# Kernel optimization log

Hardware: AMD Instinct MI355X
Metric: run time of the kernel (lower is better)

The kernel has to match this reference:

```python
import jax, jax.numpy as jnp
import numpy as np


def setup_inputs() -> dict:
    key = jax.random.key(0)
    k1, _ = jax.random.split(key)
    x = jax.random.normal(k1, (32, 64, 192, 192), dtype=jnp.float32)
    gamma = jnp.zeros((1,), dtype=jnp.float32)
    return {"x": x, "gamma": gamma}


def reference(x, gamma):
    B, C, H, W = x.shape
    q = x.reshape(B, C, H * W)                      # [B, C, N]
    # energy[b, c, d] = <q[b,c,:], q[b,d,:]>
    energy = jnp.einsum('bcn,bdn->bcd', q, q)       # [B, C, C]
    # max-subtract trick: softmax over (max - energy)
    energy_new = jnp.max(energy, axis=-1, keepdims=True) - energy
    attention = jax.nn.softmax(energy_new, axis=-1)  # [B, C, C]
    out = jnp.einsum('bcd,bdn->bcn', attention, q)   # [B, C, N]
    out = out.reshape(B, C, H, W)
    return x * (gamma[0] * out) + x
```

## Files before the change

### kernel.cpp

```cpp
#include <hip/hip_runtime.h>


#define BATCH 32
#define CH 64
#define NSP 36864

#define KSPLIT 36
#define KPER (NSP / KSPLIT)
#define BK 64

#define NB 128

using frag  = __attribute__((ext_vector_type(8))) short;
using f32x4 = __attribute__((ext_vector_type(4))) float;

__device__ inline unsigned short f2bf(float f) {
    unsigned u = __builtin_bit_cast(unsigned, f);
    unsigned r = (u + 0x7FFFu + ((u >> 16) & 1u)) >> 16;
    return (unsigned short)r;
}
__device__ inline unsigned pack2(float a, float b) {
    return (unsigned)f2bf(a) | ((unsigned)f2bf(b) << 16);
}

__global__ __launch_bounds__(256) void gram_kernel(const float* __restrict__ x,
                                                   float* __restrict__ energy) {
    const int b = blockIdx.x;
    const int kb = blockIdx.y;
    const int tid = threadIdx.x;
    const int wv = tid >> 6;
    const int lane = tid & 63;
    const int l15 = lane & 15;
    const int quad = lane >> 4;

    __shared__ unsigned short tile[CH][72];

    const float* xb = x + (size_t)b * CH * NSP + (size_t)kb * KPER;

    f32x4 acc[4];
#pragma unroll
    for (int cb = 0; cb < 4; cb++)
#pragma unroll
        for (int r = 0; r < 4; r++) acc[cb][r] = 0.f;

    for (int s = 0; s < KPER / BK; s++) {
        float4 v[4];
#pragma unroll
        for (int rep = 0; rep < 4; rep++) {
            int idx = rep * 256 + tid;
            int c = idx >> 4, kq = idx & 15;
            v[rep] = *(const float4*)&xb[(size_t)c * NSP + s * BK + kq * 4];
        }
        __syncthreads();
#pragma unroll
        for (int rep = 0; rep < 4; rep++) {
            int idx = rep * 256 + tid;
            int c = idx >> 4, kq = idx & 15;
            uint2 p;
            p.x = pack2(v[rep].x, v[rep].y);
            p.y = pack2(v[rep].z, v[rep].w);
            *(uint2*)&tile[c][kq * 4] = p;
        }
        __syncthreads();

#pragma unroll
        for (int ks = 0; ks < 2; ks++) {
            frag a = *(const frag*)&tile[wv * 16 + l15][ks * 32 + quad * 8];
#pragma unroll
            for (int cb = 0; cb < 4; cb++) {
                frag bb = *(const frag*)&tile[cb * 16 + l15][ks * 32 + quad * 8];
                acc[cb] = __builtin_amdgcn_mfma_f32_16x16x32_bf16(a, bb, acc[cb], 0, 0, 0);
            }
        }
    }

    float* eb = energy + (size_t)b * CH * CH;
#pragma unroll
    for (int cb = 0; cb < 4; cb++)
#pragma unroll
        for (int r = 0; r < 4; r++) {
            int row = wv * 16 + quad * 4 + r;
            int col = cb * 16 + l15;
            atomicAdd(&eb[row * CH + col], acc[cb][r]);
        }
}

__global__ __launch_bounds__(64) void softmax_kernel(const float* __restrict__ energy,
                                                     float* __restrict__ att) {
    const int row = blockIdx.x;
    const int d = threadIdx.x;
    float e = energy[(size_t)row * CH + d];

    float m = e;
#pragma unroll
    for (int off = 32; off > 0; off >>= 1) m = fmaxf(m, __shfl_down(m, off));
    m = __shfl(m, 0);

    float en = m - e;

    float mx = en;
#pragma unroll
    for (int off = 32; off > 0; off >>= 1) mx = fmaxf(mx, __shfl_down(mx, off));
    mx = __shfl(mx, 0);

    float ex = __expf(en - mx);
    float s = ex;
#pragma unroll
    for (int off = 32; off > 0; off >>= 1) s += __shfl_down(s, off);
    s = __shfl(s, 0);

    att[(size_t)row * CH + d] = ex / s;
}

__global__ __launch_bounds__(256) void proj_kernel(const float* __restrict__ x,
                                                   const float* __restrict__ att,
                                                   const float* __restrict__ gamma,
                                                   float* __restrict__ out) {
    const int b = blockIdx.x;
    const int n0 = blockIdx.y * NB;
    const int tid = threadIdx.x;
    const int wv = tid >> 6;
    const int lane = tid & 63;
    const int l15 = lane & 15;
    const int quad = lane >> 4;

    __shared__ float xs[CH][NB + 1];
    __shared__ unsigned short satt[CH][72];

    const float* xb = x + (size_t)b * CH * NSP;

#pragma unroll
    for (int rep = 0; rep < 4; rep++) {
        int idx = rep * 256 + tid;
        int c = idx >> 4, j = idx & 15;
        float4 v = *(const float4*)&att[(size_t)b * CH * CH + c * CH + j * 4];
        uint2 p;
        p.x = pack2(v.x, v.y);
        p.y = pack2(v.z, v.w);
        *(uint2*)&satt[c][j * 4] = p;
    }
#pragma unroll
    for (int rep = 0; rep < 8; rep++) {
        int idx = rep * 256 + tid;
        int d = idx >> 5, nq = idx & 31;
        float4 v = *(const float4*)&xb[(size_t)d * NSP + n0 + nq * 4];
        *(float4*)&xs[d][nq * 4] = v;
    }
    __syncthreads();

    const float g = gamma[0];

    f32x4 acc[2][4];
#pragma unroll
    for (int t = 0; t < 2; t++)
#pragma unroll
        for (int cb = 0; cb < 4; cb++)
#pragma unroll
            for (int r = 0; r < 4; r++) acc[t][cb][r] = 0.f;

#pragma unroll
    for (int ks = 0; ks < 2; ks++) {
        frag af[4];
#pragma unroll
        for (int cb = 0; cb < 4; cb++)
            af[cb] = *(const frag*)&satt[cb * 16 + l15][ks * 32 + quad * 8];
#pragma unroll
        for (int t = 0; t < 2; t++) {
            int n = (wv * 2 + t) * 16 + l15;
            int k0 = ks * 32 + quad * 8;
            uint4 packed;
            packed.x = pack2(xs[k0 + 0][n], xs[k0 + 1][n]);
            packed.y = pack2(xs[k0 + 2][n], xs[k0 + 3][n]);
            packed.z = pack2(xs[k0 + 4][n], xs[k0 + 5][n]);
            packed.w = pack2(xs[k0 + 6][n], xs[k0 + 7][n]);
            frag bf = __builtin_bit_cast(frag, packed);
#pragma unroll
            for (int cb = 0; cb < 4; cb++)
                acc[t][cb] = __builtin_amdgcn_mfma_f32_16x16x32_bf16(af[cb], bf, acc[t][cb], 0, 0, 0);
        }
    }

    float* ob = out + (size_t)b * CH * NSP;
#pragma unroll
    for (int t = 0; t < 2; t++) {
        int n = (wv * 2 + t) * 16 + l15;
#pragma unroll
        for (int cb = 0; cb < 4; cb++)
#pragma unroll
            for (int r = 0; r < 4; r++) {
                int c = cb * 16 + quad * 4 + r;
                float xv = xs[c][n];
                ob[(size_t)c * NSP + n0 + n] = fmaf(xv * g, acc[t][cb][r], xv);
            }
    }
}

extern "C" void kernel_launch(void* const* d_in, const int* in_sizes, int n_in,
                              void* d_out, int out_size, void* d_ws, size_t ws_size,
                              hipStream_t stream) {
    const float* x = (const float*)d_in[0];
    const float* gamma = (const float*)d_in[1];
    float* out = (float*)d_out;

    float* energy = (float*)d_ws;
    float* att = energy + (size_t)BATCH * CH * CH;

    hipMemsetAsync(energy, 0, (size_t)BATCH * CH * CH * sizeof(float), stream);

    gram_kernel<<<dim3(BATCH, KSPLIT), 256, 0, stream>>>(x, energy);
    softmax_kernel<<<BATCH * CH, 64, 0, stream>>>(energy, att);
    proj_kernel<<<dim3(BATCH, NSP / NB), 256, 0, stream>>>(x, att, gamma, out);
}
```

Before: 598.8 us.

## Prefetch next tiles in gram and proj kernels, replace atomics with partial buffers

The gram kernel doubles its K tile and loads the next tile into registers while MFMAs run on the current one. It writes per-split partial Gram matrices instead of using atomicAdd, which removes the memset; the softmax kernel sums the 36 partials. The proj kernel now walks 8 spatial chunks per block with register prefetch of the next chunk, and both kernels get occupancy hints in launch_bounds. In exchange the workspace is larger, softmax does more reads, and there is more register pressure.

```diff
diff --git a/kernel.cpp b/kernel.cpp
--- a/kernel.cpp
+++ b/kernel.cpp
@@ -7,9 +7,12 @@
 
 #define KSPLIT 36
 #define KPER (NSP / KSPLIT)
-#define BK 64
+#define BK 128
+#define SITER (KPER / BK)
 
 #define NB 128
+#define NCHUNK 8
+#define NBLKY (NSP / (NB * NCHUNK))
 
 using frag  = __attribute__((ext_vector_type(8))) short;
 using f32x4 = __attribute__((ext_vector_type(4))) float;
@@ -23,8 +26,8 @@
     return (unsigned)f2bf(a) | ((unsigned)f2bf(b) << 16);
 }
 
-__global__ __launch_bounds__(256) void gram_kernel(const float* __restrict__ x,
-                                                   float* __restrict__ energy) {
+__global__ __launch_bounds__(256, 4) void gram_kernel(const float* __restrict__ x,
+                                                      float* __restrict__ part) {
     const int b = blockIdx.x;
     const int kb = blockIdx.y;
     const int tid = threadIdx.x;
@@ -33,7 +36,7 @@
     const int l15 = lane & 15;
     const int quad = lane >> 4;
 
-    __shared__ unsigned short tile[CH][72];
+    __shared__ unsigned short tile[CH][BK + 8];
 
     const float* xb = x + (size_t)b * CH * NSP + (size_t)kb * KPER;
 
@@ -43,19 +46,20 @@
 #pragma unroll
         for (int r = 0; r < 4; r++) acc[cb][r] = 0.f;
 
-    for (int s = 0; s < KPER / BK; s++) {
-        float4 v[4];
-#pragma unroll
-        for (int rep = 0; rep < 4; rep++) {
+    float4 v[8];
+#pragma unroll
+    for (int rep = 0; rep < 8; rep++) {
+        int idx = rep * 256 + tid;
+        int c = idx >> 5, kq = idx & 31;
+        v[rep] = *(const float4*)&xb[(size_t)c * NSP + kq * 4];
+    }
+
+    for (int s = 0; s < SITER; s++) {
+        __syncthreads();
+#pragma unroll
+        for (int rep = 0; rep < 8; rep++) {
             int idx = rep * 256 + tid;
-            int c = idx >> 4, kq = idx & 15;
-            v[rep] = *(const float4*)&xb[(size_t)c * NSP + s * BK + kq * 4];
-        }
-        __syncthreads();
-#pragma unroll
-        for (int rep = 0; rep < 4; rep++) {
-            int idx = rep * 256 + tid;
-            int c = idx >> 4, kq = idx & 15;
+            int c = idx >> 5, kq = idx & 31;
             uint2 p;
             p.x = pack2(v[rep].x, v[rep].y);
             p.y = pack2(v[rep].z, v[rep].w);
@@ -63,8 +67,17 @@
         }
         __syncthreads();
 
-#pragma unroll
-        for (int ks = 0; ks < 2; ks++) {
+        if (s + 1 < SITER) {
+#pragma unroll
+            for (int rep = 0; rep < 8; rep++) {
+                int idx = rep * 256 + tid;
+                int c = idx >> 5, kq = idx & 31;
+                v[rep] = *(const float4*)&xb[(size_t)c * NSP + (s + 1) * BK + kq * 4];
+            }
+        }
+
+#pragma unroll
+        for (int ks = 0; ks < 4; ks++) {
             frag a = *(const frag*)&tile[wv * 16 + l15][ks * 32 + quad * 8];
 #pragma unroll
             for (int cb = 0; cb < 4; cb++) {
@@ -74,22 +87,26 @@
         }
     }
 
-    float* eb = energy + (size_t)b * CH * CH;
+    float* eb = part + ((size_t)kb * BATCH + b) * CH * CH;
 #pragma unroll
     for (int cb = 0; cb < 4; cb++)
 #pragma unroll
         for (int r = 0; r < 4; r++) {
             int row = wv * 16 + quad * 4 + r;
             int col = cb * 16 + l15;
-            atomicAdd(&eb[row * CH + col], acc[cb][r]);
-        }
-}
-
-__global__ __launch_bounds__(64) void softmax_kernel(const float* __restrict__ energy,
+            eb[row * CH + col] = acc[cb][r];
+        }
+}
+
+__global__ __launch_bounds__(64) void softmax_kernel(const float* __restrict__ part,
                                                      float* __restrict__ att) {
     const int row = blockIdx.x;
     const int d = threadIdx.x;
-    float e = energy[(size_t)row * CH + d];
+
+    float e = 0.f;
+#pragma unroll
+    for (int kb = 0; kb < KSPLIT; kb++)
+        e += part[(size_t)kb * (BATCH * CH * CH) + (size_t)row * CH + d];
 
     float m = e;
 #pragma unroll
@@ -112,12 +129,11 @@
     att[(size_t)row * CH + d] = ex / s;
 }
 
-__global__ __launch_bounds__(256) void proj_kernel(const float* __restrict__ x,
-                                                   const float* __restrict__ att,
-                                                   const float* __restrict__ gamma,
-                                                   float* __restrict__ out) {
+__global__ __launch_bounds__(256, 3) void proj_kernel(const float* __restrict__ x,
+                                                      const float* __restrict__ att,
+                                                      const float* __restrict__ gamma,
+                                                      float* __restrict__ out) {
     const int b = blockIdx.x;
-    const int n0 = blockIdx.y * NB;
     const int tid = threadIdx.x;
     const int wv = tid >> 6;
     const int lane = tid & 63;
@@ -128,70 +144,93 @@
     __shared__ unsigned short satt[CH][72];
 
     const float* xb = x + (size_t)b * CH * NSP;
+    float* ob = out + (size_t)b * CH * NSP;
 
 #pragma unroll
     for (int rep = 0; rep < 4; rep++) {
         int idx = rep * 256 + tid;
         int c = idx >> 4, j = idx & 15;
-        float4 v = *(const float4*)&att[(size_t)b * CH * CH + c * CH + j * 4];
+        float4 a4 = *(const float4*)&att[(size_t)b * CH * CH + c * CH + j * 4];
         uint2 p;
-        p.x = pack2(v.x, v.y);
-        p.y = pack2(v.z, v.w);
+        p.x = pack2(a4.x, a4.y);
+        p.y = pack2(a4.z, a4.w);
         *(uint2*)&satt[c][j * 4] = p;
     }
+
+    const float g = gamma[0];
+    const int nbase = blockIdx.y * (NB * NCHUNK);
+
+    float4 v[8];
 #pragma unroll
     for (int rep = 0; rep < 8; rep++) {
         int idx = rep * 256 + tid;
-        int d = idx >> 5, nq = idx & 31;
-        float4 v = *(const float4*)&xb[(size_t)d * NSP + n0 + nq * 4];
-        *(float4*)&xs[d][nq * 4] = v;
-    }
-    __syncthreads();
-
-    const float g = gamma[0];
-
-    f32x4 acc[2][4];
-#pragma unroll
-    for (int t = 0; t < 2; t++)
-#pragma unroll
-        for (int cb = 0; cb < 4; cb++)
-#pragma unroll
-            for (int r = 0; r < 4; r++) acc[t][cb][r] = 0.f;
-
-#pragma unroll
-    for (int ks = 0; ks < 2; ks++) {
-        frag af[4];
-#pragma unroll
-        for (int cb = 0; cb < 4; cb++)
-            af[cb] = *(const frag*)&satt[cb * 16 + l15][ks * 32 + quad * 8];
+        int dd = idx >> 5, nq = idx & 31;
+        v[rep] = *(const float4*)&xb[(size_t)dd * NSP + nbase + nq * 4];
+    }
+
+    for (int ch = 0; ch < NCHUNK; ch++) {
+        const int n0 = nbase + ch * NB;
+
+        __syncthreads();
+#pragma unroll
+        for (int rep = 0; rep < 8; rep++) {
+            int idx = rep * 256 + tid;
+            int dd = idx >> 5, nq = idx & 31;
+            *(float4*)&xs[dd][nq * 4] = v[rep];
+        }
+        __syncthreads();
+
+        if (ch + 1 < NCHUNK) {
+#pragma unroll
+            for (int rep = 0; rep < 8; rep++) {
+                int idx = rep * 256 + tid;
+                int dd = idx >> 5, nq = idx & 31;
+                v[rep] = *(const float4*)&xb[(size_t)dd * NSP + n0 + NB + nq * 4];
+            }
+        }
+
+        f32x4 acc[2][4];
+#pragma unroll
+        for (int t = 0; t < 2; t++)
+#pragma unroll
+            for (int cb = 0; cb < 4; cb++)
+#pragma unroll
+                for (int r = 0; r < 4; r++) acc[t][cb][r] = 0.f;
+
+#pragma unroll
+        for (int ks = 0; ks < 2; ks++) {
+            frag af[4];
+#pragma unroll
+            for (int cb = 0; cb < 4; cb++)
+                af[cb] = *(const frag*)&satt[cb * 16 + l15][ks * 32 + quad * 8];
+#pragma unroll
+            for (int t = 0; t < 2; t++) {
+                int n = (wv * 2 + t) * 16 + l15;
+                int k0 = ks * 32 + quad * 8;
+                uint4 packed;
+                packed.x = pack2(xs[k0 + 0][n], xs[k0 + 1][n]);
+                packed.y = pack2(xs[k0 + 2][n], xs[k0 + 3][n]);
+                packed.z = pack2(xs[k0 + 4][n], xs[k0 + 5][n]);
+                packed.w = pack2(xs[k0 + 6][n], xs[k0 + 7][n]);
+                frag bf = __builtin_bit_cast(frag, packed);
+#pragma unroll
+                for (int cb = 0; cb < 4; cb++)
+                    acc[t][cb] = __builtin_amdgcn_mfma_f32_16x16x32_bf16(af[cb], bf, acc[t][cb], 0, 0, 0);
+            }
+        }
+
 #pragma unroll
         for (int t = 0; t < 2; t++) {
             int n = (wv * 2 + t) * 16 + l15;
-            int k0 = ks * 32 + quad * 8;
-            uint4 packed;
-            packed.x = pack2(xs[k0 + 0][n], xs[k0 + 1][n]);
-            packed.y = pack2(xs[k0 + 2][n], xs[k0 + 3][n]);
-            packed.z = pack2(xs[k0 + 4][n], xs[k0 + 5][n]);
-            packed.w = pack2(xs[k0 + 6][n], xs[k0 + 7][n]);
-            frag bf = __builtin_bit_cast(frag, packed);
 #pragma unroll
             for (int cb = 0; cb < 4; cb++)
-                acc[t][cb] = __builtin_amdgcn_mfma_f32_16x16x32_bf16(af[cb], bf, acc[t][cb], 0, 0, 0);
-        }
-    }
-
-    float* ob = out + (size_t)b * CH * NSP;
-#pragma unroll
-    for (int t = 0; t < 2; t++) {
-        int n = (wv * 2 + t) * 16 + l15;
-#pragma unroll
-        for (int cb = 0; cb < 4; cb++)
-#pragma unroll
-            for (int r = 0; r < 4; r++) {
-                int c = cb * 16 + quad * 4 + r;
-                float xv = xs[c][n];
-                ob[(size_t)c * NSP + n0 + n] = fmaf(xv * g, acc[t][cb][r], xv);
-            }
+#pragma unroll
+                for (int r = 0; r < 4; r++) {
+                    int c = cb * 16 + quad * 4 + r;
+                    float xv = xs[c][n];
+                    ob[(size_t)c * NSP + n0 + n] = fmaf(xv * g, acc[t][cb][r], xv);
+                }
+        }
     }
 }
 
@@ -202,12 +241,10 @@
     const float* gamma = (const float*)d_in[1];
     float* out = (float*)d_out;
 
-    float* energy = (float*)d_ws;
-    float* att = energy + (size_t)BATCH * CH * CH;
-
-    hipMemsetAsync(energy, 0, (size_t)BATCH * CH * CH * sizeof(float), stream);
-
-    gram_kernel<<<dim3(BATCH, KSPLIT), 256, 0, stream>>>(x, energy);
-    softmax_kernel<<<BATCH * CH, 64, 0, stream>>>(energy, att);
-    proj_kernel<<<dim3(BATCH, NSP / NB), 256, 0, stream>>>(x, att, gamma, out);
-}
+    float* part = (float*)d_ws;
+    float* att = part + (size_t)KSPLIT * BATCH * CH * CH;
+
+    gram_kernel<<<dim3(BATCH, KSPLIT), 256, 0, stream>>>(x, part);
+    softmax_kernel<<<BATCH * CH, 64, 0, stream>>>(part, att);
+    proj_kernel<<<dim3(BATCH, NBLKY), 256, 0, stream>>>(x, att, gamma, out);
+}
```

After: 768.2 us. +28.3%, slower.
